# Kernel optimization log

Hardware: AMD Instinct MI355X
Metric: run time of the kernel (lower is better)

## Reference

```python
import jax, jax.numpy as jnp
import numpy as np

N = 100000      # nodes
E = 1600000     # edges (avg degree 16)
IN = 128        # in_channels
HID = 32        # hidden_channels per head
HEADS = 4
OUT = 64        # out_channels
NEG_SLOPE = 0.2 # PyG GATConv default leaky_relu slope


def setup_inputs() -> dict:
    key = jax.random.key(0)
    ks = jax.random.split(key, 12)
    def glorot(k, shape):
        fan = shape[0] + shape[-1]
        s = jnp.sqrt(6.0 / fan)
        return jax.random.uniform(k, shape, jnp.float32, -s, s)
    return {
        "x": jax.random.normal(ks[0], (N, IN), jnp.float32),
        "edge_index": jax.random.randint(ks[1], (2, E), 0, N, dtype=jnp.int64),
        # GATConv layer 1: in=IN, out=HID per head, heads=HEADS, concat=True
        "W1": glorot(ks[2], (IN, HEADS * HID)),
        "a_src1": glorot(ks[3], (HEADS, HID)),
        "a_dst1": glorot(ks[4], (HEADS, HID)),
        "b1": jnp.zeros((HEADS * HID,), jnp.float32),
        # GATConv layer 2: in=HEADS*HID, out=OUT, heads=1, concat=False
        "W2": glorot(ks[5], (HEADS * HID, OUT)),
        "a_src2": glorot(ks[6], (1, OUT)),
        "a_dst2": glorot(ks[7], (1, OUT)),
        "b2": jnp.zeros((OUT,), jnp.float32),
    }


def _gat_layer(x, src, dst, W, a_src, a_dst, bias, num_nodes, concat):
    """PyG-style GATConv (add_self_loops already applied to src/dst).
    x: [N, F_in]; src/dst: [E']; W: [F_in, H*C]; a_*: [H, C]."""
    H, C = a_src.shape
    h = (x @ W).reshape(-1, H, C)                       # [N, H, C]
    # per-node attention scores (avoid gathering full features for logits)
    e_src = (h * a_src[None]).sum(-1)                   # [N, H]
    e_dst = (h * a_dst[None]).sum(-1)                   # [N, H]
    logits = jax.nn.leaky_relu(e_src[src] + e_dst[dst], NEG_SLOPE)  # [E', H]
    # segment softmax over incoming edges of each destination node
    mx = jax.ops.segment_max(logits, dst, num_segments=num_nodes)   # [N, H]
    ex = jnp.exp(logits - mx[dst])                      # [E', H]
    den = jax.ops.segment_sum(ex, dst, num_segments=num_nodes)      # [N, H]
    alpha = ex / (den[dst] + 1e-16)                     # [E', H]
    # weighted message aggregation
    msg = h[src] * alpha[..., None]                     # [E', H, C]
    out = jax.ops.segment_sum(msg, dst, num_segments=num_nodes)     # [N, H, C]
    if concat:
        out = out.reshape(num_nodes, H * C)
    else:
        out = out.mean(axis=1)
    return out + bias


def reference(x, edge_index, W1, a_src1, a_dst1, b1, W2, a_src2, a_dst2, b2):
    n = x.shape[0]
    loops = jnp.arange(n, dtype=edge_index.dtype)
    src = jnp.concatenate([edge_index[0], loops])       # add self-loops (PyG default)
    dst = jnp.concatenate([edge_index[1], loops])
    # dropout layers are identity in eval mode
    h = _gat_layer(x, src, dst, W1, a_src1, a_dst1, b1, n, concat=True)
    h = jax.nn.elu(h)
    out = _gat_layer(h, src, dst, W2, a_src2, a_dst2, b2, n, concat=False)
    return out
```

## Files before the change

kernel.cpp:

```cpp
#include <hip/hip_runtime.h>
#include <cmath>

#define IN_F 128
#define NEG_SLOPE 0.2f
#define SEG 64
#define BSHIFT 7
#define NBMAX 1024
#define CHUNK 8192
#define SLOT 4096
#define LDSTRIDE 136

typedef short bfrag8 __attribute__((ext_vector_type(8)));
typedef float facc4 __attribute__((ext_vector_type(4)));

__device__ __forceinline__ int ldidx(const int* ei, int pos, int is64) {
  return is64 ? ei[2 * pos] : ei[pos];
}
__device__ __forceinline__ unsigned short f2b(float f) {
  unsigned u = __float_as_uint(f);
  u += 0x7fffu + ((u >> 16) & 1u);
  return (unsigned short)(u >> 16);
}
__device__ __forceinline__ float b2f_lo(unsigned u) { return __uint_as_float(u << 16); }
__device__ __forceinline__ float b2f_hi(unsigned u) { return __uint_as_float(u & 0xffff0000u); }
__device__ __forceinline__ void wave_lds_fence() {
  asm volatile("s_waitcnt lgkmcnt(0)" ::: "memory");
}
__device__ __forceinline__ float leaky(float l) { return fmaxf(l, NEG_SLOPE * l); }
__device__ __forceinline__ float elu(float o) { return o > 0.f ? o : __expf(o) - 1.f; }

__global__ __launch_bounds__(256) void detect_kernel(const int* __restrict__ ei, int E, int* __restrict__ flag) {
  __shared__ int red[256];
  int acc = 0;
  int limit = E < 4096 ? E : 4096;
  for (int j = threadIdx.x; j < limit; j += 256) acc |= ei[2 * j + 1];
  red[threadIdx.x] = acc;
  __syncthreads();
  for (int s = 128; s > 0; s >>= 1) {
    if ((int)threadIdx.x < s) red[threadIdx.x] |= red[threadIdx.x + s];
    __syncthreads();
  }
  if (threadIdx.x == 0) *flag = (red[0] == 0) ? 1 : 0;
}

__global__ __launch_bounds__(1024) void binit_kernel(int* __restrict__ bcur, int NB) {
  int tid = threadIdx.x;
  if (tid < NB) bcur[tid] = tid * SLOT;
}

__global__ __launch_bounds__(256) void bscatter_kernel(const int* __restrict__ ei, int E, int Etot,
                                                       const int* __restrict__ flag, int NB,
                                                       int* __restrict__ bcur, unsigned* __restrict__ ebuf) {
  __shared__ int hcnt[NBMAX];
  __shared__ int hcur[NBMAX];
  int tid = threadIdx.x;
  int base = blockIdx.x * CHUNK;
  int cnt = Etot - base; if (cnt > CHUNK) cnt = CHUNK;
  int is64 = *flag;
  for (int i = tid; i < NB; i += 256) hcnt[i] = 0;
  __syncthreads();
  for (int i = tid; i < cnt; i += 256) {
    int e = base + i;
    int d = (e < E) ? ldidx(ei, E + e, is64) : (e - E);
    atomicAdd(&hcnt[d >> BSHIFT], 1);
  }
  __syncthreads();
  for (int i = tid; i < NB; i += 256) {
    int c = hcnt[i];
    hcur[i] = c ? atomicAdd(&bcur[i], c) : 0;
  }
  __syncthreads();
  for (int i = tid; i < cnt; i += 256) {
    int e = base + i;
    int s, d;
    if (e < E) { s = ldidx(ei, e, is64); d = ldidx(ei, E + e, is64); }
    else       { s = e - E; d = s; }
    int pos = atomicAdd(&hcur[d >> BSHIFT], 1);
    ebuf[pos] = ((unsigned)s << 7) | ((unsigned)d & 127u);
  }
}

__global__ __launch_bounds__(256) void bcsr_kernel(const int* __restrict__ bcur, const unsigned* __restrict__ ebuf,
                                                   int* __restrict__ rowptr, int* __restrict__ rowdeg,
                                                   int* __restrict__ csr, int N, int NB) {
  __shared__ int cnt[128];
  __shared__ int cur[128];
  __shared__ int w0sum;
  int tid = threadIdx.x;
  int b = blockIdx.x;
  int lo = b * SLOT, hi = bcur[b];
  int node0 = b << BSHIFT;
  int nn = N - node0; if (nn > 128) nn = 128;
  if (tid < 128) cnt[tid] = 0;
  __syncthreads();
  for (int i = lo + tid; i < hi; i += 256) {
    atomicAdd(&cnt[ebuf[i] & 127u], 1);
  }
  __syncthreads();
  int v = 0, incl = 0;
  if (tid < 128) {
    v = cnt[tid];
    incl = v;
    int lane = tid & 63;
    #pragma unroll
    for (int off = 1; off < 64; off <<= 1) { int t = __shfl_up(incl, off); if (lane >= off) incl += t; }
    if (tid == 63) w0sum = incl;
  }
  __syncthreads();
  if (tid < 128) {
    if (tid >= 64) incl += w0sum;
    int excl = incl - v;
    cur[tid] = excl;
    if (tid < nn) {
      rowptr[node0 + tid] = lo + excl;
      rowdeg[node0 + tid] = v;
    }
  }
  __syncthreads();
  for (int i = lo + tid; i < hi; i += 256) {
    unsigned pr = ebuf[i];
    int p = atomicAdd(&cur[pr & 127u], 1);
    csr[lo + p] = (int)(pr >> 7);
  }
}

__global__ __launch_bounds__(256) void gemm1_kernel(
    const float* __restrict__ x, const float* __restrict__ W,
    const float* __restrict__ asr, const float* __restrict__ ads,
    unsigned short* __restrict__ h1b, float* __restrict__ es, float* __restrict__ ed,
    int N) {
  __shared__ short Wt[128 * LDSTRIDE];
  __shared__ short As[64 * LDSTRIDE];
  int tid = threadIdx.x;
  int row0 = blockIdx.x * 64;
  int lane = tid & 63, wv = tid >> 6;
  int m2 = lane & 15, quad = lane >> 4;

  for (int i = tid; i < 128 * 128; i += 256) {
    int k = i >> 7, c = i & 127;
    Wt[c * LDSTRIDE + k] = (short)f2b(W[i]);
  }
  for (int idx = tid; idx < 64 * 16; idx += 256) {
    int r = idx >> 4, ch = idx & 15;
    int n = row0 + r;
    bfrag8 sv;
    if (n < N) {
      float4 v0 = *(const float4*)&x[(size_t)n * 128 + ch * 8];
      float4 v1 = *(const float4*)&x[(size_t)n * 128 + ch * 8 + 4];
      sv[0] = (short)f2b(v0.x); sv[1] = (short)f2b(v0.y);
      sv[2] = (short)f2b(v0.z); sv[3] = (short)f2b(v0.w);
      sv[4] = (short)f2b(v1.x); sv[5] = (short)f2b(v1.y);
      sv[6] = (short)f2b(v1.z); sv[7] = (short)f2b(v1.w);
    } else {
      sv = (bfrag8)0;
    }
    *(bfrag8*)&As[r * LDSTRIDE + ch * 8] = sv;
  }
  __syncthreads();

  facc4 acc[8] = {};
  const short* Abase = &As[(wv * 16 + m2) * LDSTRIDE];
  #pragma unroll
  for (int ks = 0; ks < 4; ++ks) {
    int k = ks * 32 + quad * 8;
    bfrag8 af = *(const bfrag8*)&Abase[k];
    #pragma unroll
    for (int t = 0; t < 8; ++t) {
      bfrag8 bf = *(const bfrag8*)&Wt[(t * 16 + m2) * LDSTRIDE + k];
      acc[t] = __builtin_amdgcn_mfma_f32_16x16x32_bf16(af, bf, acc[t], 0, 0, 0);
    }
  }

  float av[8], bv[8];
  #pragma unroll
  for (int t = 0; t < 8; ++t) {
    int ai = (t >> 1) * 32 + (t & 1) * 16 + m2;
    av[t] = asr[ai]; bv[t] = ads[ai];
  }
  #pragma unroll
  for (int r = 0; r < 4; ++r) {
    int n = row0 + wv * 16 + quad * 4 + r;
    bool valid = (n < N);
    if (valid) {
      #pragma unroll
      for (int t = 0; t < 8; ++t)
        h1b[(size_t)n * 128 + t * 16 + m2] = f2b(acc[t][r]);
    }
    #pragma unroll
    for (int h = 0; h < 4; ++h) {
      float ps = acc[2 * h][r] * av[2 * h] + acc[2 * h + 1][r] * av[2 * h + 1];
      float pd = acc[2 * h][r] * bv[2 * h] + acc[2 * h + 1][r] * bv[2 * h + 1];
      ps += __shfl_xor(ps, 1); ps += __shfl_xor(ps, 2); ps += __shfl_xor(ps, 4); ps += __shfl_xor(ps, 8);
      pd += __shfl_xor(pd, 1); pd += __shfl_xor(pd, 2); pd += __shfl_xor(pd, 4); pd += __shfl_xor(pd, 8);
      if (valid && m2 == 0) {
        es[(size_t)n * 4 + h] = ps;
        ed[(size_t)n * 4 + h] = pd;
      }
    }
  }
}

__global__ __launch_bounds__(256) void gemm2_kernel(
    const unsigned short* __restrict__ xb, const float* __restrict__ W,
    const float* __restrict__ asr, const float* __restrict__ ads,
    unsigned short* __restrict__ h2b, float* __restrict__ es, float* __restrict__ ed,
    int N) {
  __shared__ short Wt[64 * LDSTRIDE];
  __shared__ short As[64 * LDSTRIDE];
  int tid = threadIdx.x;
  int row0 = blockIdx.x * 64;
  int lane = tid & 63, wv = tid >> 6;
  int m2 = lane & 15, quad = lane >> 4;

  for (int i = tid; i < 128 * 64; i += 256) {
    int k = i >> 6, c = i & 63;
    Wt[c * LDSTRIDE + k] = (short)f2b(W[i]);
  }
  for (int idx = tid; idx < 64 * 16; idx += 256) {
    int r = idx >> 4, ch = idx & 15;
    int n = row0 + r;
    uint4 u = (n < N) ? *(const uint4*)&xb[(size_t)n * 128 + ch * 8]
                      : make_uint4(0, 0, 0, 0);
    *(uint4*)&As[r * LDSTRIDE + ch * 8] = u;
  }
  __syncthreads();

  facc4 acc[4] = {};
  const short* Abase = &As[(wv * 16 + m2) * LDSTRIDE];
  #pragma unroll
  for (int ks = 0; ks < 4; ++ks) {
    int k = ks * 32 + quad * 8;
    bfrag8 af = *(const bfrag8*)&Abase[k];
    #pragma unroll
    for (int t = 0; t < 4; ++t) {
      bfrag8 bf = *(const bfrag8*)&Wt[(t * 16 + m2) * LDSTRIDE + k];
      acc[t] = __builtin_amdgcn_mfma_f32_16x16x32_bf16(af, bf, acc[t], 0, 0, 0);
    }
  }

  float av[4], bv[4];
  #pragma unroll
  for (int t = 0; t < 4; ++t) {
    av[t] = asr[t * 16 + m2]; bv[t] = ads[t * 16 + m2];
  }
  #pragma unroll
  for (int r = 0; r < 4; ++r) {
    int n = row0 + wv * 16 + quad * 4 + r;
    bool valid = (n < N);
    if (valid) {
      #pragma unroll
      for (int t = 0; t < 4; ++t)
        h2b[(size_t)n * 64 + t * 16 + m2] = f2b(acc[t][r]);
    }
    float ps = acc[0][r] * av[0] + acc[1][r] * av[1] + acc[2][r] * av[2] + acc[3][r] * av[3];
    float pd = acc[0][r] * bv[0] + acc[1][r] * bv[1] + acc[2][r] * bv[2] + acc[3][r] * bv[3];
    ps += __shfl_xor(ps, 1); ps += __shfl_xor(ps, 2); ps += __shfl_xor(ps, 4); ps += __shfl_xor(ps, 8);
    pd += __shfl_xor(pd, 1); pd += __shfl_xor(pd, 2); pd += __shfl_xor(pd, 4); pd += __shfl_xor(pd, 8);
    if (valid && m2 == 0) { es[n] = ps; ed[n] = pd; }
  }
}

__global__ __launch_bounds__(256) void agg1_kernel(
    const int* __restrict__ rowptr, const int* __restrict__ rowdeg, const int* __restrict__ csr,
    const float* __restrict__ es, const float* __restrict__ ed,
    const unsigned short* __restrict__ h1b, const float* __restrict__ bias1,
    unsigned short* __restrict__ hmidb, int N) {
  __shared__ float lds_a[4][4][4][SEG + 4];
  __shared__ int   lds_s[4][4][SEG + 4];
  int tid = threadIdx.x;
  int wv = tid >> 6, lane = tid & 63;
  int sub = lane >> 4, sj = lane & 15;
  int nbase = blockIdx.x * 16 + wv * 4;
  int n = nbase + sub;
  bool nvalid = (n < N);
  int start = 0, len = 0;
  if (nvalid) { start = rowptr[n]; len = rowdeg[n]; }
  int lenc = (len <= SEG) ? len : 0;

  float4 edv = nvalid ? ((const float4*)ed)[n] : make_float4(0.f, 0.f, 0.f, 0.f);
  float l[4][4];
  float mx = -1e30f;
  #pragma unroll
  for (int it = 0; it < 4; ++it) {
    int j = sj + it * 16;
    if (j < lenc) {
      int s = csr[start + j];
      lds_s[wv][sub][j] = s;
      float4 ev = ((const float4*)es)[s];
      float l0 = leaky(ev.x + edv.x);
      float l1 = leaky(ev.y + edv.y);
      float l2 = leaky(ev.z + edv.z);
      float l3 = leaky(ev.w + edv.w);
      l[it][0] = l0; l[it][1] = l1; l[it][2] = l2; l[it][3] = l3;
      mx = fmaxf(mx, fmaxf(fmaxf(l0, l1), fmaxf(l2, l3)));
    } else {
      l[it][0] = -1e30f; l[it][1] = -1e30f; l[it][2] = -1e30f; l[it][3] = -1e30f;
    }
  }
  #pragma unroll
  for (int off = 1; off < 16; off <<= 1) mx = fmaxf(mx, __shfl_xor(mx, off));

  float s0 = 0.f, s1 = 0.f, s2 = 0.f, s3 = 0.f;
  #pragma unroll
  for (int it = 0; it < 4; ++it) {
    float p0 = __expf(l[it][0] - mx);
    float p1 = __expf(l[it][1] - mx);
    float p2 = __expf(l[it][2] - mx);
    float p3 = __expf(l[it][3] - mx);
    l[it][0] = p0; l[it][1] = p1; l[it][2] = p2; l[it][3] = p3;
    s0 += p0; s1 += p1; s2 += p2; s3 += p3;
  }
  #pragma unroll
  for (int off = 1; off < 16; off <<= 1) {
    s0 += __shfl_xor(s0, off); s1 += __shfl_xor(s1, off);
    s2 += __shfl_xor(s2, off); s3 += __shfl_xor(s3, off);
  }
  float i0 = __builtin_amdgcn_rcpf(s0 + 1e-16f);
  float i1 = __builtin_amdgcn_rcpf(s1 + 1e-16f);
  float i2 = __builtin_amdgcn_rcpf(s2 + 1e-16f);
  float i3 = __builtin_amdgcn_rcpf(s3 + 1e-16f);
  #pragma unroll
  for (int it = 0; it < 4; ++it) {
    int j = sj + it * 16;
    if (j < lenc) {
      lds_a[wv][sub][0][j] = l[it][0] * i0;
      lds_a[wv][sub][1][j] = l[it][1] * i1;
      lds_a[wv][sub][2][j] = l[it][2] * i2;
      lds_a[wv][sub][3][j] = l[it][3] * i3;
    }
  }
  if (sj == 0) {
    int lenp1 = (lenc + 3) & ~3;
    for (int t = lenc; t < lenp1; ++t) {
      lds_s[wv][sub][t] = 0;
      lds_a[wv][sub][0][t] = 0.f; lds_a[wv][sub][1][t] = 0.f;
      lds_a[wv][sub][2][t] = 0.f; lds_a[wv][sub][3][t] = 0.f;
    }
  }
  wave_lds_fence();

  int fl = lane & 15, eidx = lane >> 4, hd = fl >> 2;
  const uint4* hrow = (const uint4*)h1b;
  #pragma unroll 1
  for (int i = 0; i < 4; ++i) {
    int lenC = __shfl(lenc, i << 4);
    if (lenC == 0) continue;
    int nI = nbase + i;
    const int* sP = &lds_s[wv][i][0];
    const float* aP = &lds_a[wv][i][hd][0];
    int lenp = (lenC + 3) & ~3;
    float c0 = 0.f, c1 = 0.f, c2 = 0.f, c3 = 0.f, c4 = 0.f, c5 = 0.f, c6 = 0.f, c7 = 0.f;
    float d0 = 0.f, d1 = 0.f, d2 = 0.f, d3 = 0.f, d4 = 0.f, d5 = 0.f, d6 = 0.f, d7 = 0.f;
    int g = 0;
    for (; g + 8 <= lenp; g += 8) {
      int sA = sP[g + eidx], sB = sP[g + 4 + eidx];
      float wA = aP[g + eidx];
      float wB = aP[g + 4 + eidx];
      uint4 uA = hrow[(size_t)sA * 16 + fl];
      uint4 uB = hrow[(size_t)sB * 16 + fl];
      c0 = fmaf(b2f_lo(uA.x), wA, c0); c1 = fmaf(b2f_hi(uA.x), wA, c1);
      c2 = fmaf(b2f_lo(uA.y), wA, c2); c3 = fmaf(b2f_hi(uA.y), wA, c3);
      c4 = fmaf(b2f_lo(uA.z), wA, c4); c5 = fmaf(b2f_hi(uA.z), wA, c5);
      c6 = fmaf(b2f_lo(uA.w), wA, c6); c7 = fmaf(b2f_hi(uA.w), wA, c7);
      d0 = fmaf(b2f_lo(uB.x), wB, d0); d1 = fmaf(b2f_hi(uB.x), wB, d1);
      d2 = fmaf(b2f_lo(uB.y), wB, d2); d3 = fmaf(b2f_hi(uB.y), wB, d3);
      d4 = fmaf(b2f_lo(uB.z), wB, d4); d5 = fmaf(b2f_hi(uB.z), wB, d5);
      d6 = fmaf(b2f_lo(uB.w), wB, d6); d7 = fmaf(b2f_hi(uB.w), wB, d7);
    }
    if (g < lenp) {
      int sA = sP[g + eidx];
      float wA = aP[g + eidx];
      uint4 uA = hrow[(size_t)sA * 16 + fl];
      c0 = fmaf(b2f_lo(uA.x), wA, c0); c1 = fmaf(b2f_hi(uA.x), wA, c1);
      c2 = fmaf(b2f_lo(uA.y), wA, c2); c3 = fmaf(b2f_hi(uA.y), wA, c3);
      c4 = fmaf(b2f_lo(uA.z), wA, c4); c5 = fmaf(b2f_hi(uA.z), wA, c5);
      c6 = fmaf(b2f_lo(uA.w), wA, c6); c7 = fmaf(b2f_hi(uA.w), wA, c7);
    }
    c0 += d0; c1 += d1; c2 += d2; c3 += d3; c4 += d4; c5 += d5; c6 += d6; c7 += d7;
    c0 += __shfl_xor(c0, 16); c1 += __shfl_xor(c1, 16); c2 += __shfl_xor(c2, 16); c3 += __shfl_xor(c3, 16);
    c4 += __shfl_xor(c4, 16); c5 += __shfl_xor(c5, 16); c6 += __shfl_xor(c6, 16); c7 += __shfl_xor(c7, 16);
    c0 += __shfl_xor(c0, 32); c1 += __shfl_xor(c1, 32); c2 += __shfl_xor(c2, 32); c3 += __shfl_xor(c3, 32);
    c4 += __shfl_xor(c4, 32); c5 += __shfl_xor(c5, 32); c6 += __shfl_xor(c6, 32); c7 += __shfl_xor(c7, 32);
    if (eidx == 0) {
      float4 ba = *(const float4*)&bias1[fl * 8];
      float4 bb = *(const float4*)&bias1[fl * 8 + 4];
      float o0 = elu(c0 + ba.x), o1 = elu(c1 + ba.y), o2 = elu(c2 + ba.z), o3 = elu(c3 + ba.w);
      float o4 = elu(c4 + bb.x), o5 = elu(c5 + bb.y), o6 = elu(c6 + bb.z), o7 = elu(c7 + bb.w);
      uint4 pk;
      pk.x = (unsigned)f2b(o0) | ((unsigned)f2b(o1) << 16);
      pk.y = (unsigned)f2b(o2) | ((unsigned)f2b(o3) << 16);
      pk.z = (unsigned)f2b(o4) | ((unsigned)f2b(o5) << 16);
      pk.w = (unsigned)f2b(o6) | ((unsigned)f2b(o7) << 16);
      ((uint4*)hmidb)[(size_t)nI * 16 + fl] = pk;
    }
  }

  #pragma unroll 1
  for (int i = 0; i < 4; ++i) {
    int lenF = __shfl(len, i << 4);
    if (lenF <= SEG) continue;
    int stF = __shfl(start, i << 4);
    int nI = nbase + i;
    float4 ed4 = ((const float4*)ed)[nI];
    int f = lane * 2, hh = lane >> 4;
    const unsigned* h32 = (const unsigned*)h1b;
    float m0 = -1e30f, m1 = -1e30f, m2 = -1e30f, m3 = -1e30f;
    for (int j = stF + lane; j < stF + lenF; j += 64) {
      int s = csr[j];
      float4 ev = ((const float4*)es)[s];
      m0 = fmaxf(m0, leaky(ev.x + ed4.x)); m1 = fmaxf(m1, leaky(ev.y + ed4.y));
      m2 = fmaxf(m2, leaky(ev.z + ed4.z)); m3 = fmaxf(m3, leaky(ev.w + ed4.w));
    }
    #pragma unroll
    for (int off = 32; off; off >>= 1) {
      m0 = fmaxf(m0, __shfl_xor(m0, off)); m1 = fmaxf(m1, __shfl_xor(m1, off));
      m2 = fmaxf(m2, __shfl_xor(m2, off)); m3 = fmaxf(m3, __shfl_xor(m3, off));
    }
    float t0 = 0.f, t1 = 0.f, t2 = 0.f, t3 = 0.f;
    for (int j = stF + lane; j < stF + lenF; j += 64) {
      int s = csr[j];
      float4 ev = ((const float4*)es)[s];
      t0 += __expf(leaky(ev.x + ed4.x) - m0); t1 += __expf(leaky(ev.y + ed4.y) - m1);
      t2 += __expf(leaky(ev.z + ed4.z) - m2); t3 += __expf(leaky(ev.w + ed4.w) - m3);
    }
    #pragma unroll
    for (int off = 32; off; off >>= 1) {
      t0 += __shfl_xor(t0, off); t1 += __shfl_xor(t1, off);
      t2 += __shfl_xor(t2, off); t3 += __shfl_xor(t3, off);
    }
    float j0 = 1.f / (t0 + 1e-16f), j1 = 1.f / (t1 + 1e-16f);
    float j2 = 1.f / (t2 + 1e-16f), j3 = 1.f / (t3 + 1e-16f);
    float edh = (hh & 2) ? ((hh & 1) ? ed4.w : ed4.z) : ((hh & 1) ? ed4.y : ed4.x);
    float mh  = (hh & 2) ? ((hh & 1) ? m3 : m2) : ((hh & 1) ? m1 : m0);
    float ih  = (hh & 2) ? ((hh & 1) ? j3 : j2) : ((hh & 1) ? j1 : j0);
    float ax = 0.f, ay = 0.f;
    for (int j = stF; j < stF + lenF; ++j) {
      int s = csr[j];
      float lv = leaky(es[(size_t)s * 4 + hh] + edh);
      float a = __expf(lv - mh) * ih;
      unsigned u = h32[(size_t)s * 64 + lane];
      ax = fmaf(b2f_lo(u), a, ax);
      ay = fmaf(b2f_hi(u), a, ay);
    }
    float o0 = elu(ax + bias1[f]), o1 = elu(ay + bias1[f + 1]);
    unsigned packed = (unsigned)f2b(o0) | ((unsigned)f2b(o1) << 16);
    ((unsigned*)hmidb)[(size_t)nI * 64 + lane] = packed;
  }
}

__global__ __launch_bounds__(256) void agg2_kernel(
    const int* __restrict__ rowptr, const int* __restrict__ rowdeg, const int* __restrict__ csr,
    const float* __restrict__ es, const float* __restrict__ ed,
    const unsigned short* __restrict__ h2b, const float* __restrict__ bias2,
    float* __restrict__ out, int N) {
  __shared__ float lds_a[4][4][SEG + 8];
  __shared__ int   lds_s[4][4][SEG + 8];
  int tid = threadIdx.x;
  int wv = tid >> 6, lane = tid & 63;
  int sub = lane >> 4, sj = lane & 15;
  int nbase = blockIdx.x * 16 + wv * 4;
  int n = nbase + sub;
  bool nvalid = (n < N);
  int start = 0, len = 0;
  if (nvalid) { start = rowptr[n]; len = rowdeg[n]; }
  int lenc = (len <= SEG) ? len : 0;

  float edv = nvalid ? ed[n] : 0.f;
  float l[4];
  float mx = -1e30f;
  #pragma unroll
  for (int it = 0; it < 4; ++it) {
    int j = sj + it * 16;
    if (j < lenc) {
      int s = csr[start + j];
      lds_s[wv][sub][j] = s;
      float lv = leaky(es[s] + edv);
      l[it] = lv;
      mx = fmaxf(mx, lv);
    } else {
      l[it] = -1e30f;
    }
  }
  #pragma unroll
  for (int off = 1; off < 16; off <<= 1) mx = fmaxf(mx, __shfl_xor(mx, off));
  float sm = 0.f;
  #pragma unroll
  for (int it = 0; it < 4; ++it) {
    float p = __expf(l[it] - mx);
    l[it] = p;
    sm += p;
  }
  #pragma unroll
  for (int off = 1; off < 16; off <<= 1) sm += __shfl_xor(sm, off);
  float inv = __builtin_amdgcn_rcpf(sm + 1e-16f);
  #pragma unroll
  for (int it = 0; it < 4; ++it) {
    int j = sj + it * 16;
    if (j < lenc) lds_a[wv][sub][j] = l[it] * inv;
  }
  if (sj == 0) {
    int lenp1 = (lenc + 7) & ~7;
    for (int t = lenc; t < lenp1; ++t) {
      lds_s[wv][sub][t] = 0;
      lds_a[wv][sub][t] = 0.f;
    }
  }
  wave_lds_fence();

  int fl = lane & 7, eidx = lane >> 3;
  const uint4* hrow = (const uint4*)h2b;
  #pragma unroll 1
  for (int i = 0; i < 4; ++i) {
    int lenC = __shfl(lenc, i << 4);
    if (lenC == 0) continue;
    int nI = nbase + i;
    const float* aP = &lds_a[wv][i][0];
    const int*   sP = &lds_s[wv][i][0];
    int lenp = (lenC + 7) & ~7;
    float c0 = 0.f, c1 = 0.f, c2 = 0.f, c3 = 0.f, c4 = 0.f, c5 = 0.f, c6 = 0.f, c7 = 0.f;
    float d0 = 0.f, d1 = 0.f, d2 = 0.f, d3 = 0.f, d4 = 0.f, d5 = 0.f, d6 = 0.f, d7 = 0.f;
    int g = 0;
    for (; g + 16 <= lenp; g += 16) {
      int sA = sP[g + eidx],   sB = sP[g + 8 + eidx];
      float wA = aP[g + eidx], wB = aP[g + 8 + eidx];
      uint4 uA = hrow[(size_t)sA * 8 + fl];
      uint4 uB = hrow[(size_t)sB * 8 + fl];
      c0 = fmaf(b2f_lo(uA.x), wA, c0); c1 = fmaf(b2f_hi(uA.x), wA, c1);
      c2 = fmaf(b2f_lo(uA.y), wA, c2); c3 = fmaf(b2f_hi(uA.y), wA, c3);
      c4 = fmaf(b2f_lo(uA.z), wA, c4); c5 = fmaf(b2f_hi(uA.z), wA, c5);
      c6 = fmaf(b2f_lo(uA.w), wA, c6); c7 = fmaf(b2f_hi(uA.w), wA, c7);
      d0 = fmaf(b2f_lo(uB.x), wB, d0); d1 = fmaf(b2f_hi(uB.x), wB, d1);
      d2 = fmaf(b2f_lo(uB.y), wB, d2); d3 = fmaf(b2f_hi(uB.y), wB, d3);
      d4 = fmaf(b2f_lo(uB.z), wB, d4); d5 = fmaf(b2f_hi(uB.z), wB, d5);
      d6 = fmaf(b2f_lo(uB.w), wB, d6); d7 = fmaf(b2f_hi(uB.w), wB, d7);
    }
    if (g < lenp) {
      int sA = sP[g + eidx];
      float wA = aP[g + eidx];
      uint4 uA = hrow[(size_t)sA * 8 + fl];
      c0 = fmaf(b2f_lo(uA.x), wA, c0); c1 = fmaf(b2f_hi(uA.x), wA, c1);
      c2 = fmaf(b2f_lo(uA.y), wA, c2); c3 = fmaf(b2f_hi(uA.y), wA, c3);
      c4 = fmaf(b2f_lo(uA.z), wA, c4); c5 = fmaf(b2f_hi(uA.z), wA, c5);
      c6 = fmaf(b2f_lo(uA.w), wA, c6); c7 = fmaf(b2f_hi(uA.w), wA, c7);
    }
    c0 += d0; c1 += d1; c2 += d2; c3 += d3; c4 += d4; c5 += d5; c6 += d6; c7 += d7;
    c0 += __shfl_xor(c0, 8);  c1 += __shfl_xor(c1, 8);  c2 += __shfl_xor(c2, 8);  c3 += __shfl_xor(c3, 8);
    c4 += __shfl_xor(c4, 8);  c5 += __shfl_xor(c5, 8);  c6 += __shfl_xor(c6, 8);  c7 += __shfl_xor(c7, 8);
    c0 += __shfl_xor(c0, 16); c1 += __shfl_xor(c1, 16); c2 += __shfl_xor(c2, 16); c3 += __shfl_xor(c3, 16);
    c4 += __shfl_xor(c4, 16); c5 += __shfl_xor(c5, 16); c6 += __shfl_xor(c6, 16); c7 += __shfl_xor(c7, 16);
    c0 += __shfl_xor(c0, 32); c1 += __shfl_xor(c1, 32); c2 += __shfl_xor(c2, 32); c3 += __shfl_xor(c3, 32);
    c4 += __shfl_xor(c4, 32); c5 += __shfl_xor(c5, 32); c6 += __shfl_xor(c6, 32); c7 += __shfl_xor(c7, 32);
    if (eidx == 0) {
      float4 ba = *(const float4*)&bias2[fl * 8];
      float4 bb = *(const float4*)&bias2[fl * 8 + 4];
      ((float4*)out)[(size_t)nI * 16 + fl * 2]     = make_float4(c0 + ba.x, c1 + ba.y, c2 + ba.z, c3 + ba.w);
      ((float4*)out)[(size_t)nI * 16 + fl * 2 + 1] = make_float4(c4 + bb.x, c5 + bb.y, c6 + bb.z, c7 + bb.w);
    }
  }

  #pragma unroll 1
  for (int i = 0; i < 4; ++i) {
    int lenF = __shfl(len, i << 4);
    if (lenF <= SEG) continue;
    int stF = __shfl(start, i << 4);
    int nI = nbase + i;
    float edF = ed[nI];
    float m = -1e30f;
    for (int j = stF + lane; j < stF + lenF; j += 64) {
      m = fmaxf(m, leaky(es[csr[j]] + edF));
    }
    #pragma unroll
    for (int off = 32; off; off >>= 1) m = fmaxf(m, __shfl_xor(m, off));
    float t = 0.f;
    for (int j = stF + lane; j < stF + lenF; j += 64) {
      t += __expf(leaky(es[csr[j]] + edF) - m);
    }
    #pragma unroll
    for (int off = 32; off; off >>= 1) t += __shfl_xor(t, off);
    float iv = 1.f / (t + 1e-16f);
    float acc = 0.f;
    for (int j = stF; j < stF + lenF; ++j) {
      int s = csr[j];
      float a = __expf(leaky(es[s] + edF) - m) * iv;
      float v = __uint_as_float(((unsigned)h2b[(size_t)s * 64 + lane]) << 16);
      acc = fmaf(v, a, acc);
    }
    out[(size_t)nI * 64 + lane] = acc + bias2[lane];
  }
}

extern "C" void kernel_launch(void* const* d_in, const int* in_sizes, int n_in,
                              void* d_out, int out_size, void* d_ws, size_t ws_size,
                              hipStream_t stream) {
  const float* x   = (const float*)d_in[0];
  const int*   ei  = (const int*)d_in[1];
  const float* W1  = (const float*)d_in[2];
  const float* as1 = (const float*)d_in[3];
  const float* ad1 = (const float*)d_in[4];
  const float* b1  = (const float*)d_in[5];
  const float* W2  = (const float*)d_in[6];
  const float* as2 = (const float*)d_in[7];
  const float* ad2 = (const float*)d_in[8];
  const float* b2  = (const float*)d_in[9];
  float* out = (float*)d_out;

  int N = in_sizes[0] / IN_F;
  int E = in_sizes[1] / 2;
  int Etot = E + N;
  int NB = (N + 127) >> BSHIFT;

  char* p = (char*)d_ws;
  auto carve = [&](size_t bytes) -> char* {
    char* r = p;
    p += (bytes + 255) & ~(size_t)255;
    return r;
  };
  int* flag     = (int*)carve(4);
  int* bcur     = (int*)carve((size_t)NBMAX * 4);
  unsigned* ebuf = (unsigned*)carve((size_t)NB * SLOT * 4);
  int* rowptr   = (int*)carve((size_t)(N + 1) * 4);
  int* rowdeg   = (int*)carve((size_t)(N + 1) * 4);
  int* csr      = (int*)carve((size_t)NB * SLOT * 4);
  float* es1    = (float*)carve((size_t)N * 4 * 4);
  float* ed1    = (float*)carve((size_t)N * 4 * 4);
  float* es2    = (float*)carve((size_t)N * 4);
  float* ed2    = (float*)carve((size_t)N * 4);
  unsigned short* h1b   = (unsigned short*)carve((size_t)N * 128 * 2);
  unsigned short* hmidb = (unsigned short*)carve((size_t)N * 128 * 2);
  unsigned short* h2b   = (unsigned short*)carve((size_t)N * 64 * 2);

  int nchunk = (Etot + CHUNK - 1) / CHUNK;
  detect_kernel<<<1, 256, 0, stream>>>(ei, E, flag);
  binit_kernel<<<1, 1024, 0, stream>>>(bcur, NB);
  bscatter_kernel<<<nchunk, 256, 0, stream>>>(ei, E, Etot, flag, NB, bcur, ebuf);
  bcsr_kernel<<<NB, 256, 0, stream>>>(bcur, ebuf, rowptr, rowdeg, csr, N, NB);
  gemm1_kernel<<<(N + 63) / 64, 256, 0, stream>>>(x, W1, as1, ad1, h1b, es1, ed1, N);
  agg1_kernel<<<(N + 15) / 16, 256, 0, stream>>>(rowptr, rowdeg, csr, es1, ed1, h1b, b1, hmidb, N);
  gemm2_kernel<<<(N + 63) / 64, 256, 0, stream>>>(hmidb, W2, as2, ad2, h2b, es2, ed2, N);
  agg2_kernel<<<(N + 15) / 16, 256, 0, stream>>>(rowptr, rowdeg, csr, es2, ed2, h2b, b2, out, N);
}
```

Before: 333.2 us.

## Merge prologue kernels, pre-convert weights once, stage CSR in LDS, packed FMA

```diff
diff --git a/kernel.cpp b/kernel.cpp
--- a/kernel.cpp
+++ b/kernel.cpp
@@ -6,12 +6,13 @@
 #define SEG 64
 #define BSHIFT 7
 #define NBMAX 1024
-#define CHUNK 8192
+#define CHUNK 2048
 #define SLOT 4096
 #define LDSTRIDE 136
 
 typedef short bfrag8 __attribute__((ext_vector_type(8)));
 typedef float facc4 __attribute__((ext_vector_type(4)));
+typedef float v2f __attribute__((ext_vector_type(2)));
 
 __device__ __forceinline__ int ldidx(const int* ei, int pos, int is64) {
   return is64 ? ei[2 * pos] : ei[pos];
@@ -23,29 +24,46 @@
 }
 __device__ __forceinline__ float b2f_lo(unsigned u) { return __uint_as_float(u << 16); }
 __device__ __forceinline__ float b2f_hi(unsigned u) { return __uint_as_float(u & 0xffff0000u); }
+__device__ __forceinline__ v2f b2f2(unsigned u) {
+  v2f r; r.x = b2f_lo(u); r.y = b2f_hi(u); return r;
+}
 __device__ __forceinline__ void wave_lds_fence() {
   asm volatile("s_waitcnt lgkmcnt(0)" ::: "memory");
 }
 __device__ __forceinline__ float leaky(float l) { return fmaxf(l, NEG_SLOPE * l); }
 __device__ __forceinline__ float elu(float o) { return o > 0.f ? o : __expf(o) - 1.f; }
 
-__global__ __launch_bounds__(256) void detect_kernel(const int* __restrict__ ei, int E, int* __restrict__ flag) {
-  __shared__ int red[256];
-  int acc = 0;
-  int limit = E < 4096 ? E : 4096;
-  for (int j = threadIdx.x; j < limit; j += 256) acc |= ei[2 * j + 1];
-  red[threadIdx.x] = acc;
-  __syncthreads();
-  for (int s = 128; s > 0; s >>= 1) {
-    if ((int)threadIdx.x < s) red[threadIdx.x] |= red[threadIdx.x + s];
+__global__ __launch_bounds__(256) void prologue_kernel(
+    const int* __restrict__ ei, int E, int* __restrict__ flag,
+    int* __restrict__ bcur, int NB,
+    const float* __restrict__ W1, const float* __restrict__ W2,
+    unsigned short* __restrict__ Wt1g, unsigned short* __restrict__ Wt2g) {
+  int b = blockIdx.x, tid = threadIdx.x;
+  if (b == 0) {
+    __shared__ int red[256];
+    int acc = 0;
+    int limit = E < 4096 ? E : 4096;
+    for (int j = tid; j < limit; j += 256) acc |= ei[2 * j + 1];
+    red[tid] = acc;
     __syncthreads();
-  }
-  if (threadIdx.x == 0) *flag = (red[0] == 0) ? 1 : 0;
-}
-
-__global__ __launch_bounds__(1024) void binit_kernel(int* __restrict__ bcur, int NB) {
-  int tid = threadIdx.x;
-  if (tid < NB) bcur[tid] = tid * SLOT;
+    for (int s = 128; s > 0; s >>= 1) {
+      if (tid < s) red[tid] |= red[tid + s];
+      __syncthreads();
+    }
+    if (tid == 0) *flag = (red[0] == 0) ? 1 : 0;
+  } else if (b == 1) {
+    for (int i = tid; i < NB; i += 256) bcur[i] = i * SLOT;
+  } else if (b < 8) {
+    for (int i = (b - 2) * 256 + tid; i < 128 * 128; i += 6 * 256) {
+      int k = i >> 7, c = i & 127;
+      Wt1g[c * 128 + k] = f2b(W1[i]);
+    }
+  } else {
+    for (int i = (b - 8) * 256 + tid; i < 128 * 64; i += 6 * 256) {
+      int k = i >> 6, c = i & 63;
+      Wt2g[c * 128 + k] = f2b(W2[i]);
+    }
+  }
 }
 
 __global__ __launch_bounds__(256) void bscatter_kernel(const int* __restrict__ ei, int E, int Etot,
@@ -83,18 +101,22 @@
 __global__ __launch_bounds__(256) void bcsr_kernel(const int* __restrict__ bcur, const unsigned* __restrict__ ebuf,
                                                    int* __restrict__ rowptr, int* __restrict__ rowdeg,
                                                    int* __restrict__ csr, int N, int NB) {
+  __shared__ unsigned se[SLOT];
+  __shared__ int scsr[SLOT];
   __shared__ int cnt[128];
   __shared__ int cur[128];
   __shared__ int w0sum;
   int tid = threadIdx.x;
   int b = blockIdx.x;
   int lo = b * SLOT, hi = bcur[b];
+  int fill = hi - lo;
   int node0 = b << BSHIFT;
   int nn = N - node0; if (nn > 128) nn = 128;
   if (tid < 128) cnt[tid] = 0;
-  __syncthreads();
-  for (int i = lo + tid; i < hi; i += 256) {
-    atomicAdd(&cnt[ebuf[i] & 127u], 1);
+  for (int i = tid; i < fill; i += 256) se[i] = ebuf[lo + i];
+  __syncthreads();
+  for (int i = tid; i < fill; i += 256) {
+    atomicAdd(&cnt[se[i] & 127u], 1);
   }
   __syncthreads();
   int v = 0, incl = 0;
@@ -117,15 +139,17 @@
     }
   }
   __syncthreads();
-  for (int i = lo + tid; i < hi; i += 256) {
-    unsigned pr = ebuf[i];
+  for (int i = tid; i < fill; i += 256) {
+    unsigned pr = se[i];
     int p = atomicAdd(&cur[pr & 127u], 1);
-    csr[lo + p] = (int)(pr >> 7);
-  }
+    scsr[p] = (int)(pr >> 7);
+  }
+  __syncthreads();
+  for (int i = tid; i < fill; i += 256) csr[lo + i] = scsr[i];
 }
 
 __global__ __launch_bounds__(256) void gemm1_kernel(
-    const float* __restrict__ x, const float* __restrict__ W,
+    const float* __restrict__ x, const unsigned short* __restrict__ Wt1g,
     const float* __restrict__ asr, const float* __restrict__ ads,
     unsigned short* __restrict__ h1b, float* __restrict__ es, float* __restrict__ ed,
     int N) {
@@ -136,9 +160,9 @@
   int lane = tid & 63, wv = tid >> 6;
   int m2 = lane & 15, quad = lane >> 4;
 
-  for (int i = tid; i < 128 * 128; i += 256) {
-    int k = i >> 7, c = i & 127;
-    Wt[c * LDSTRIDE + k] = (short)f2b(W[i]);
+  for (int i = tid; i < 128 * 16; i += 256) {
+    int c = i >> 4, ch = i & 15;
+    *(uint4*)&Wt[c * LDSTRIDE + ch * 8] = *(const uint4*)&Wt1g[c * 128 + ch * 8];
   }
   for (int idx = tid; idx < 64 * 16; idx += 256) {
     int r = idx >> 4, ch = idx & 15;
@@ -201,7 +225,7 @@
 }
 
 __global__ __launch_bounds__(256) void gemm2_kernel(
-    const unsigned short* __restrict__ xb, const float* __restrict__ W,
+    const unsigned short* __restrict__ xb, const unsigned short* __restrict__ Wt2g,
     const float* __restrict__ asr, const float* __restrict__ ads,
     unsigned short* __restrict__ h2b, float* __restrict__ es, float* __restrict__ ed,
     int N) {
@@ -212,9 +236,9 @@
   int lane = tid & 63, wv = tid >> 6;
   int m2 = lane & 15, quad = lane >> 4;
 
-  for (int i = tid; i < 128 * 64; i += 256) {
-    int k = i >> 6, c = i & 63;
-    Wt[c * LDSTRIDE + k] = (short)f2b(W[i]);
+  for (int i = tid; i < 64 * 16; i += 256) {
+    int c = i >> 4, ch = i & 15;
+    *(uint4*)&Wt[c * LDSTRIDE + ch * 8] = *(const uint4*)&Wt2g[c * 128 + ch * 8];
   }
   for (int idx = tid; idx < 64 * 16; idx += 256) {
     int r = idx >> 4, ch = idx & 15;
@@ -349,8 +373,8 @@
     const int* sP = &lds_s[wv][i][0];
     const float* aP = &lds_a[wv][i][hd][0];
     int lenp = (lenC + 3) & ~3;
-    float c0 = 0.f, c1 = 0.f, c2 = 0.f, c3 = 0.f, c4 = 0.f, c5 = 0.f, c6 = 0.f, c7 = 0.f;
-    float d0 = 0.f, d1 = 0.f, d2 = 0.f, d3 = 0.f, d4 = 0.f, d5 = 0.f, d6 = 0.f, d7 = 0.f;
+    v2f C0 = {0.f, 0.f}, C1 = {0.f, 0.f}, C2 = {0.f, 0.f}, C3 = {0.f, 0.f};
+    v2f D0 = {0.f, 0.f}, D1 = {0.f, 0.f}, D2 = {0.f, 0.f}, D3 = {0.f, 0.f};
     int g = 0;
     for (; g + 8 <= lenp; g += 8) {
       int sA = sP[g + eidx], sB = sP[g + 4 + eidx];
@@ -358,25 +382,29 @@
       float wB = aP[g + 4 + eidx];
       uint4 uA = hrow[(size_t)sA * 16 + fl];
       uint4 uB = hrow[(size_t)sB * 16 + fl];
-      c0 = fmaf(b2f_lo(uA.x), wA, c0); c1 = fmaf(b2f_hi(uA.x), wA, c1);
-      c2 = fmaf(b2f_lo(uA.y), wA, c2); c3 = fmaf(b2f_hi(uA.y), wA, c3);
-      c4 = fmaf(b2f_lo(uA.z), wA, c4); c5 = fmaf(b2f_hi(uA.z), wA, c5);
-      c6 = fmaf(b2f_lo(uA.w), wA, c6); c7 = fmaf(b2f_hi(uA.w), wA, c7);
-      d0 = fmaf(b2f_lo(uB.x), wB, d0); d1 = fmaf(b2f_hi(uB.x), wB, d1);
-      d2 = fmaf(b2f_lo(uB.y), wB, d2); d3 = fmaf(b2f_hi(uB.y), wB, d3);
-      d4 = fmaf(b2f_lo(uB.z), wB, d4); d5 = fmaf(b2f_hi(uB.z), wB, d5);
-      d6 = fmaf(b2f_lo(uB.w), wB, d6); d7 = fmaf(b2f_hi(uB.w), wB, d7);
+      v2f wA2 = {wA, wA}, wB2 = {wB, wB};
+      C0 = __builtin_elementwise_fma(b2f2(uA.x), wA2, C0);
+      C1 = __builtin_elementwise_fma(b2f2(uA.y), wA2, C1);
+      C2 = __builtin_elementwise_fma(b2f2(uA.z), wA2, C2);
+      C3 = __builtin_elementwise_fma(b2f2(uA.w), wA2, C3);
+      D0 = __builtin_elementwise_fma(b2f2(uB.x), wB2, D0);
+      D1 = __builtin_elementwise_fma(b2f2(uB.y), wB2, D1);
+      D2 = __builtin_elementwise_fma(b2f2(uB.z), wB2, D2);
+      D3 = __builtin_elementwise_fma(b2f2(uB.w), wB2, D3);
     }
     if (g < lenp) {
       int sA = sP[g + eidx];
       float wA = aP[g + eidx];
       uint4 uA = hrow[(size_t)sA * 16 + fl];
-      c0 = fmaf(b2f_lo(uA.x), wA, c0); c1 = fmaf(b2f_hi(uA.x), wA, c1);
-      c2 = fmaf(b2f_lo(uA.y), wA, c2); c3 = fmaf(b2f_hi(uA.y), wA, c3);
-      c4 = fmaf(b2f_lo(uA.z), wA, c4); c5 = fmaf(b2f_hi(uA.z), wA, c5);
-      c6 = fmaf(b2f_lo(uA.w), wA, c6); c7 = fmaf(b2f_hi(uA.w), wA, c7);
-    }
-    c0 += d0; c1 += d1; c2 += d2; c3 += d3; c4 += d4; c5 += d5; c6 += d6; c7 += d7;
+      v2f wA2 = {wA, wA};
+      C0 = __builtin_elementwise_fma(b2f2(uA.x), wA2, C0);
+      C1 = __builtin_elementwise_fma(b2f2(uA.y), wA2, C1);
+      C2 = __builtin_elementwise_fma(b2f2(uA.z), wA2, C2);
+      C3 = __builtin_elementwise_fma(b2f2(uA.w), wA2, C3);
+    }
+    C0 += D0; C1 += D1; C2 += D2; C3 += D3;
+    float c0 = C0.x, c1 = C0.y, c2 = C1.x, c3 = C1.y;
+    float c4 = C2.x, c5 = C2.y, c6 = C3.x, c7 = C3.y;
     c0 += __shfl_xor(c0, 16); c1 += __shfl_xor(c1, 16); c2 += __shfl_xor(c2, 16); c3 += __shfl_xor(c3, 16);
     c4 += __shfl_xor(c4, 16); c5 += __shfl_xor(c5, 16); c6 += __shfl_xor(c6, 16); c7 += __shfl_xor(c7, 16);
     c0 += __shfl_xor(c0, 32); c1 += __shfl_xor(c1, 32); c2 += __shfl_xor(c2, 32); c3 += __shfl_xor(c3, 32);
@@ -517,33 +545,37 @@
     const float* aP = &lds_a[wv][i][0];
     const int*   sP = &lds_s[wv][i][0];
     int lenp = (lenC + 7) & ~7;
-    float c0 = 0.f, c1 = 0.f, c2 = 0.f, c3 = 0.f, c4 = 0.f, c5 = 0.f, c6 = 0.f, c7 = 0.f;
-    float d0 = 0.f, d1 = 0.f, d2 = 0.f, d3 = 0.f, d4 = 0.f, d5 = 0.f, d6 = 0.f, d7 = 0.f;
+    v2f C0 = {0.f, 0.f}, C1 = {0.f, 0.f}, C2 = {0.f, 0.f}, C3 = {0.f, 0.f};
+    v2f D0 = {0.f, 0.f}, D1 = {0.f, 0.f}, D2 = {0.f, 0.f}, D3 = {0.f, 0.f};
     int g = 0;
     for (; g + 16 <= lenp; g += 16) {
       int sA = sP[g + eidx],   sB = sP[g + 8 + eidx];
       float wA = aP[g + eidx], wB = aP[g + 8 + eidx];
       uint4 uA = hrow[(size_t)sA * 8 + fl];
       uint4 uB = hrow[(size_t)sB * 8 + fl];
-      c0 = fmaf(b2f_lo(uA.x), wA, c0); c1 = fmaf(b2f_hi(uA.x), wA, c1);
-      c2 = fmaf(b2f_lo(uA.y), wA, c2); c3 = fmaf(b2f_hi(uA.y), wA, c3);
-      c4 = fmaf(b2f_lo(uA.z), wA, c4); c5 = fmaf(b2f_hi(uA.z), wA, c5);
-      c6 = fmaf(b2f_lo(uA.w), wA, c6); c7 = fmaf(b2f_hi(uA.w), wA, c7);
-      d0 = fmaf(b2f_lo(uB.x), wB, d0); d1 = fmaf(b2f_hi(uB.x), wB, d1);
-      d2 = fmaf(b2f_lo(uB.y), wB, d2); d3 = fmaf(b2f_hi(uB.y), wB, d3);
-      d4 = fmaf(b2f_lo(uB.z), wB, d4); d5 = fmaf(b2f_hi(uB.z), wB, d5);
-      d6 = fmaf(b2f_lo(uB.w), wB, d6); d7 = fmaf(b2f_hi(uB.w), wB, d7);
+      v2f wA2 = {wA, wA}, wB2 = {wB, wB};
+      C0 = __builtin_elementwise_fma(b2f2(uA.x), wA2, C0);
+      C1 = __builtin_elementwise_fma(b2f2(uA.y), wA2, C1);
+      C2 = __builtin_elementwise_fma(b2f2(uA.z), wA2, C2);
+      C3 = __builtin_elementwise_fma(b2f2(uA.w), wA2, C3);
+      D0 = __builtin_elementwise_fma(b2f2(uB.x), wB2, D0);
+      D1 = __builtin_elementwise_fma(b2f2(uB.y), wB2, D1);
+      D2 = __builtin_elementwise_fma(b2f2(uB.z), wB2, D2);
+      D3 = __builtin_elementwise_fma(b2f2(uB.w), wB2, D3);
     }
     if (g < lenp) {
       int sA = sP[g + eidx];
       float wA = aP[g + eidx];
       uint4 uA = hrow[(size_t)sA * 8 + fl];
-      c0 = fmaf(b2f_lo(uA.x), wA, c0); c1 = fmaf(b2f_hi(uA.x), wA, c1);
-      c2 = fmaf(b2f_lo(uA.y), wA, c2); c3 = fmaf(b2f_hi(uA.y), wA, c3);
-      c4 = fmaf(b2f_lo(uA.z), wA, c4); c5 = fmaf(b2f_hi(uA.z), wA, c5);
-      c6 = fmaf(b2f_lo(uA.w), wA, c6); c7 = fmaf(b2f_hi(uA.w), wA, c7);
-    }
-    c0 += d0; c1 += d1; c2 += d2; c3 += d3; c4 += d4; c5 += d5; c6 += d6; c7 += d7;
+      v2f wA2 = {wA, wA};
+      C0 = __builtin_elementwise_fma(b2f2(uA.x), wA2, C0);
+      C1 = __builtin_elementwise_fma(b2f2(uA.y), wA2, C1);
+      C2 = __builtin_elementwise_fma(b2f2(uA.z), wA2, C2);
+      C3 = __builtin_elementwise_fma(b2f2(uA.w), wA2, C3);
+    }
+    C0 += D0; C1 += D1; C2 += D2; C3 += D3;
+    float c0 = C0.x, c1 = C0.y, c2 = C1.x, c3 = C1.y;
+    float c4 = C2.x, c5 = C2.y, c6 = C3.x, c7 = C3.y;
     c0 += __shfl_xor(c0, 8);  c1 += __shfl_xor(c1, 8);  c2 += __shfl_xor(c2, 8);  c3 += __shfl_xor(c3, 8);
     c4 += __shfl_xor(c4, 8);  c5 += __shfl_xor(c5, 8);  c6 += __shfl_xor(c6, 8);  c7 += __shfl_xor(c7, 8);
     c0 += __shfl_xor(c0, 16); c1 += __shfl_xor(c1, 16); c2 += __shfl_xor(c2, 16); c3 += __shfl_xor(c3, 16);
@@ -617,6 +649,8 @@
   };
   int* flag     = (int*)carve(4);
   int* bcur     = (int*)carve((size_t)NBMAX * 4);
+  unsigned short* Wt1g = (unsigned short*)carve(128 * 128 * 2);
+  unsigned short* Wt2g = (unsigned short*)carve(64 * 128 * 2);
   unsigned* ebuf = (unsigned*)carve((size_t)NB * SLOT * 4);
   int* rowptr   = (int*)carve((size_t)(N + 1) * 4);
   int* rowdeg   = (int*)carve((size_t)(N + 1) * 4);
@@ -630,12 +664,11 @@
   unsigned short* h2b   = (unsigned short*)carve((size_t)N * 64 * 2);
 
   int nchunk = (Etot + CHUNK - 1) / CHUNK;
-  detect_kernel<<<1, 256, 0, stream>>>(ei, E, flag);
-  binit_kernel<<<1, 1024, 0, stream>>>(bcur, NB);
+  prologue_kernel<<<14, 256, 0, stream>>>(ei, E, flag, bcur, NB, W1, W2, Wt1g, Wt2g);
   bscatter_kernel<<<nchunk, 256, 0, stream>>>(ei, E, Etot, flag, NB, bcur, ebuf);
   bcsr_kernel<<<NB, 256, 0, stream>>>(bcur, ebuf, rowptr, rowdeg, csr, N, NB);
-  gemm1_kernel<<<(N + 63) / 64, 256, 0, stream>>>(x, W1, as1, ad1, h1b, es1, ed1, N);
+  gemm1_kernel<<<(N + 63) / 64, 256, 0, stream>>>(x, Wt1g, as1, ad1, h1b, es1, ed1, N);
   agg1_kernel<<<(N + 15) / 16, 256, 0, stream>>>(rowptr, rowdeg, csr, es1, ed1, h1b, b1, hmidb, N);
-  gemm2_kernel<<<(N + 63) / 64, 256, 0, stream>>>(hmidb, W2, as2, ad2, h2b, es2, ed2, N);
+  gemm2_kernel<<<(N + 63) / 64, 256, 0, stream>>>(hmidb, Wt2g, as2, ad2, h2b, es2, ed2, N);
   agg2_kernel<<<(N + 15) / 16, 256, 0, stream>>>(rowptr, rowdeg, csr, es2, ed2, h2b, b2, out, N);
 }
```

New measurement: 320.2 us. -3.9%, faster.
